# Performance work log

Measured on AMD Instinct MI355X. Metric: run time of the kernel, lower is better.

The kernel has to match this reference:

```python
import jax, jax.numpy as jnp
import numpy as np

D_MODEL = 1024
D_STATE = 64


def setup_inputs() -> dict:
    key = jax.random.key(0)
    k_x, k_a, k_b, k_c, k_d = jax.random.split(key, 5)
    x = jax.random.normal(k_x, (4, 4096, D_MODEL), dtype=jnp.float32)
    # parameter init mirrors _init_parameters
    A_diag = jax.random.uniform(k_a, (D_STATE,), minval=-0.5, maxval=0.5, dtype=jnp.float32)
    def xavier(k, shape):
        fan_in, fan_out = shape
        limit = float(np.sqrt(6.0 / (fan_in + fan_out)))
        return jax.random.uniform(k, shape, minval=-limit, maxval=limit, dtype=jnp.float32)
    B = xavier(k_b, (D_MODEL, D_STATE))
    C = xavier(k_c, (D_STATE, D_MODEL))
    D = xavier(k_d, (D_MODEL, D_MODEL)) * 0.1
    return {"x": x, "A_diag": A_diag, "B": B, "C": C, "D": D}


def reference(x, A_diag, B, C, D):
    # h_t = sigmoid(A_diag) * h_{t-1} + x_t @ B ; y_t = h_t @ C + x_t @ D
    # dropout is identity in eval mode.
    a = jax.nn.sigmoid(A_diag)                      # [S_state]
    u = jnp.einsum('btd,ds->bts', x, B)             # precompute input drive [B,T,S]

    def step(h, u_t):                               # h: [B,S], u_t: [B,S]
        h = a * h + u_t
        return h, h

    h0 = jnp.zeros((x.shape[0], A_diag.shape[0]), dtype=x.dtype)
    _, hs = jax.lax.scan(step, h0, jnp.swapaxes(u, 0, 1))  # hs: [T,B,S]
    hs = jnp.swapaxes(hs, 0, 1)                            # [B,T,S]
    y = jnp.einsum('bts,sd->btd', hs, C) + jnp.einsum('btd,de->bte', x, D)
    return y
```

## Files before the change

kernel.cpp:

```cpp
#include <hip/hip_runtime.h>
#include <hip/hip_bf16.h>

using bf16x8 = __attribute__((ext_vector_type(8))) __bf16;
using f32x4  = __attribute__((ext_vector_type(4))) float;

#define MTOT   16384
#define DMODEL 1024
#define DSTATE 64
#define KBIG   1088

__device__ __forceinline__ ushort f2b(float f) {
  __hip_bfloat16 h = __float2bfloat16(f);
  return *reinterpret_cast<ushort*>(&h);
}

__device__ __forceinline__ void gld_lds16(const ushort* g, const char* l) {
  using gptr_t = const __attribute__((address_space(1))) uint32_t*;
  using lptr_t = __attribute__((address_space(3))) uint32_t*;
  __builtin_amdgcn_global_load_lds(
      reinterpret_cast<gptr_t>(reinterpret_cast<uintptr_t>(g)),
      reinterpret_cast<lptr_t>(static_cast<uint32_t>(reinterpret_cast<uintptr_t>(l))),
      16, 0, 0);
}

#define BARRIER() do { asm volatile("" ::: "memory"); __builtin_amdgcn_s_barrier(); asm volatile("" ::: "memory"); } while (0)
#define VMCNT8() asm volatile("s_waitcnt vmcnt(8)" ::: "memory")
#define VMCNT0() asm volatile("s_waitcnt vmcnt(0)" ::: "memory")

__global__ __launch_bounds__(256) void prep_wb(const float* __restrict__ A_diag,
    const float* __restrict__ B, const float* __restrict__ C, const float* __restrict__ D,
    ushort* __restrict__ Wt, ushort* __restrict__ Btu, float* __restrict__ aSig) {
  __shared__ float tile[64][65];
  int bid = blockIdx.x;
  int tid = threadIdx.x;
  int r = tid >> 2;
  if (bid < 272) {
    int bk = bid % 17, bn = bid / 17;
    int k0 = bk * 64, n0 = bn * 64;
    const float* srow = (k0 + r < DSTATE)
        ? (C + (size_t)(k0 + r) * DMODEL + n0)
        : (D + (size_t)(k0 + r - DSTATE) * DMODEL + n0);
#pragma unroll
    for (int it = 0; it < 4; ++it) {
      int c4 = (tid & 3) + it * 4;
      float4 v = *reinterpret_cast<const float4*>(srow + c4 * 4);
      tile[r][c4 * 4 + 0] = v.x; tile[r][c4 * 4 + 1] = v.y;
      tile[r][c4 * 4 + 2] = v.z; tile[r][c4 * 4 + 3] = v.w;
    }
    __syncthreads();
#pragma unroll
    for (int it = 0; it < 2; ++it) {
      int gq = (tid & 3) + it * 4;
      ushort o[8];
#pragma unroll
      for (int j = 0; j < 8; ++j) o[j] = f2b(tile[gq * 8 + j][r]);
      *reinterpret_cast<uint4*>(&Wt[(size_t)(n0 + r) * KBIG + k0 + gq * 8]) =
          *reinterpret_cast<uint4*>(o);
    }
  } else {
    int k0 = (bid - 272) * 64;
    const float* srow = B + (size_t)(k0 + r) * DSTATE;
#pragma unroll
    for (int it = 0; it < 4; ++it) {
      int c4 = (tid & 3) + it * 4;
      float4 v = *reinterpret_cast<const float4*>(srow + c4 * 4);
      tile[r][c4 * 4 + 0] = v.x; tile[r][c4 * 4 + 1] = v.y;
      tile[r][c4 * 4 + 2] = v.z; tile[r][c4 * 4 + 3] = v.w;
    }
    __syncthreads();
#pragma unroll
    for (int it = 0; it < 2; ++it) {
      int gq = (tid & 3) + it * 4;
      ushort o[8];
#pragma unroll
      for (int j = 0; j < 8; ++j) o[j] = f2b(tile[gq * 8 + j][r]);
      *reinterpret_cast<uint4*>(&Btu[(size_t)r * DMODEL + k0 + gq * 8]) =
          *reinterpret_cast<uint4*>(o);
    }
    if (bid == 272 && tid < DSTATE) aSig[tid] = 1.0f / (1.0f + expf(-A_diag[tid]));
  }
}

__global__ __launch_bounds__(256) void fused_xu(const float* __restrict__ x,
    const ushort* __restrict__ Btu, const float* __restrict__ aSig,
    ushort* __restrict__ Z, float* __restrict__ Uloc, float* __restrict__ carry) {
  __shared__ ushort As[16][136];
  __shared__ float  Ul[16][68];
  int tid = threadIdx.x;
  int w = tid >> 6, lane = tid & 63;
  int l16 = lane & 15, lh = lane >> 4;
  int row0 = blockIdx.x * 16;
  int r = tid >> 4, kq = tid & 15;

  f32x4 acc = {};
  const float* srcBase = x + (size_t)(row0 + r) * 1024 + kq * 8;
  float4 xv0 = *reinterpret_cast<const float4*>(srcBase);
  float4 xv1 = *reinterpret_cast<const float4*>(srcBase + 4);
  for (int c = 0; c < 8; ++c) {
    int k0 = c * 128;
    ushort o[8] = {f2b(xv0.x), f2b(xv0.y), f2b(xv0.z), f2b(xv0.w),
                   f2b(xv1.x), f2b(xv1.y), f2b(xv1.z), f2b(xv1.w)};
    uint4 pk = *reinterpret_cast<uint4*>(o);
    *reinterpret_cast<uint4*>(&Z[(size_t)(row0 + r) * KBIG + DSTATE + k0 + kq * 8]) = pk;
    *reinterpret_cast<uint4*>(&As[r][kq * 8]) = pk;
    __syncthreads();
    if (c < 7) {
      const float* src = srcBase + k0 + 128;
      xv0 = *reinterpret_cast<const float4*>(src);
      xv1 = *reinterpret_cast<const float4*>(src + 4);
    }
#pragma unroll
    for (int ks = 0; ks < 4; ++ks) {
      bf16x8 af = *reinterpret_cast<const bf16x8*>(&As[l16][ks * 32 + lh * 8]);
      bf16x8 bf = *reinterpret_cast<const bf16x8*>(
          &Btu[(size_t)(w * 16 + l16) * 1024 + k0 + ks * 32 + lh * 8]);
      acc = __builtin_amdgcn_mfma_f32_16x16x32_bf16(af, bf, acc, 0, 0, 0);
    }
    __syncthreads();
  }
#pragma unroll
  for (int j = 0; j < 4; ++j)
    Ul[lh * 4 + j][w * 16 + l16] = acc[j];
  __syncthreads();
  if (w == 0) {
    int g = blockIdx.x;
    float as = aSig[lane];
    float h = 0.0f;
#pragma unroll
    for (int i = 0; i < 16; ++i) {
      h = fmaf(as, h, Ul[i][lane]);
      Uloc[(size_t)(g * 16 + i) * 64 + lane] = h;
    }
    carry[(size_t)g * 64 + lane] = h;
  }
}

__global__ __launch_bounds__(128) void scan_fix2(const float* __restrict__ aSig,
    const float* __restrict__ Uloc, const float* __restrict__ carry,
    ushort* __restrict__ Z) {
  int w = threadIdx.x >> 6, s = threadIdx.x & 63;
  int g = blockIdx.x * 2 + w;
  int b = g >> 8, c = g & 255;
  float as = aSig[s];
  float aL = as;
#pragma unroll
  for (int q = 0; q < 4; ++q) aL *= aL;
  const float* cb = carry + ((size_t)b << 8) * 64 + s;
  float H = 0.0f;
  for (int c0 = 0; c0 < 256; c0 += 16) {
    if (c0 >= c) break;
    float v[16];
#pragma unroll
    for (int i = 0; i < 16; ++i) v[i] = cb[(size_t)(c0 + i) * 64];
#pragma unroll
    for (int i = 0; i < 16; ++i)
      if (c0 + i < c) H = fmaf(aL, H, v[i]);
  }
  float p = as;
  size_t ubase = (size_t)g * 16 * 64 + s;
  size_t zbase = (size_t)(g * 16) * KBIG + s;
#pragma unroll
  for (int i = 0; i < 16; ++i) {
    float h = fmaf(p, H, Uloc[ubase + (size_t)i * 64]);
    p *= as;
    Z[zbase + (size_t)i * KBIG] = f2b(h);
  }
}

__global__ __launch_bounds__(256, 2) void gemm128(const ushort* __restrict__ A, int lda,
                                                  const ushort* __restrict__ Bt, int ldb,
                                                  float* __restrict__ Cc, int ldc, int K) {
  extern __shared__ __align__(128) char smem[];
  const int tid = threadIdx.x;
  const int wid = tid >> 6, lane = tid & 63;
  const int wm = wid >> 1, wn = wid & 1;
  const int l16 = lane & 15, lh = lane >> 4;

  int bid = blockIdx.x;
  int swz = (bid & 7) * ((int)gridDim.x >> 3) + (bid >> 3);
  const int bmRow = (swz >> 3) * 128;
  const int bnCol = (swz & 7) * 128;
  const int NT = K / 64;

  const int cswz = ((lh ^ (l16 & 7)) << 4);
  const int sRow = lane >> 3;
  const int sCol = (((lane & 7) ^ (lane >> 3)) << 3);

  const ushort* aBase = A + (size_t)(bmRow + wid * 8 + sRow) * lda + sCol;
  const ushort* bBase = Bt + (size_t)(bnCol + wid * 8 + sRow) * ldb + sCol;

  f32x4 acc[4][4] = {};
  bf16x8 aR[8], bR[8];

  auto stageA = [&](int buf, int t) {
    const ushort* g = aBase + (size_t)t * 64;
    char* d = smem + buf * 32768 + (wid * 8) * 128;
#pragma unroll
    for (int h = 0; h < 4; ++h)
      gld_lds16(g + (size_t)(h * 32) * lda, d + h * 32 * 128);
  };
  auto stageB = [&](int buf, int t) {
    const ushort* g = bBase + (size_t)t * 64;
    char* d = smem + buf * 32768 + 16384 + (wid * 8) * 128;
#pragma unroll
    for (int h = 0; h < 4; ++h)
      gld_lds16(g + (size_t)(h * 32) * ldb, d + h * 32 * 128);
  };
  auto readA = [&](int buf) {
#pragma unroll
    for (int m = 0; m < 4; ++m)
#pragma unroll
      for (int ks = 0; ks < 2; ++ks)
        aR[m * 2 + ks] = *reinterpret_cast<const bf16x8*>(
            smem + buf * 32768 + (wm * 64 + m * 16 + l16) * 128 + (cswz ^ (ks * 64)));
  };
  auto readB = [&](int buf) {
#pragma unroll
    for (int n = 0; n < 4; ++n)
#pragma unroll
      for (int ks = 0; ks < 2; ++ks)
        bR[n * 2 + ks] = *reinterpret_cast<const bf16x8*>(
            smem + buf * 32768 + 16384 + (wn * 64 + n * 16 + l16) * 128 + (cswz ^ (ks * 64)));
  };

  stageA(0, 0); stageB(0, 0);
  stageA(1, 1); stageB(1, 1);
  VMCNT8();
  BARRIER();

  for (int t = 0; t < NT; ++t) {
    const int buf = t & 1;
    const bool st2 = (t + 2 < NT);
    readA(buf); readB(buf);
    BARRIER();
    if (st2) { stageA(buf, t + 2); stageB(buf, t + 2); }
    __builtin_amdgcn_s_setprio(1);
#pragma unroll
    for (int ks = 0; ks < 2; ++ks)
#pragma unroll
      for (int m = 0; m < 4; ++m)
#pragma unroll
        for (int n = 0; n < 4; ++n)
          acc[m][n] = __builtin_amdgcn_mfma_f32_16x16x32_bf16(
              aR[m * 2 + ks], bR[n * 2 + ks], acc[m][n], 0, 0, 0);
    __builtin_amdgcn_s_setprio(0);
    if (st2) { VMCNT8(); } else { VMCNT0(); }
    BARRIER();
  }

#pragma unroll
  for (int m = 0; m < 4; ++m)
#pragma unroll
    for (int n = 0; n < 4; ++n)
#pragma unroll
      for (int j = 0; j < 4; ++j) {
        int r = bmRow + wm * 64 + m * 16 + lh * 4 + j;
        int c = bnCol + wn * 64 + n * 16 + l16;
        Cc[(size_t)r * ldc + c] = acc[m][n][j];
      }
}

extern "C" void kernel_launch(void* const* d_in, const int* in_sizes, int n_in,
                              void* d_out, int out_size, void* d_ws, size_t ws_size,
                              hipStream_t stream) {
  const float* x      = (const float*)d_in[0];
  const float* A_diag = (const float*)d_in[1];
  const float* B      = (const float*)d_in[2];
  const float* C      = (const float*)d_in[3];
  const float* D      = (const float*)d_in[4];
  float* y = (float*)d_out;

  char* w = (char*)d_ws;
  ushort* Z     = (ushort*)(w);
  ushort* Wt    = (ushort*)(w + 35651584);
  ushort* Btu   = (ushort*)(w + 37879808);
  float*  Uloc  = (float*) (w + 38010880);
  float*  carry = (float*) (w + 42205184);
  float*  aSig  = (float*) (w + 42467328);

  (void)hipFuncSetAttribute(reinterpret_cast<const void*>(&gemm128),
                            hipFuncAttributeMaxDynamicSharedMemorySize, 65536);

  prep_wb<<<dim3(288), dim3(256), 0, stream>>>(A_diag, B, C, D, Wt, Btu, aSig);
  fused_xu<<<dim3(1024), dim3(256), 0, stream>>>(x, Btu, aSig, Z, Uloc, carry);
  scan_fix2<<<dim3(512), dim3(128), 0, stream>>>(aSig, Uloc, carry, Z);
  gemm128<<<dim3(128 * 8), dim3(256), 65536, stream>>>(Z, KBIG, Wt, KBIG, y, DMODEL, KBIG);
}
```

Measured before the change: 82.71 us.

## Replace 128x128 GEMM with 256x256 tile, 8-wave ping-pong pipelined kernel

The final GEMM moves from 128x128 tiles with 4 waves to 256x256 tiles with 8 waves per block, using 128KB of LDS. It splits each K-step into four quadrant MFMA phases, and the half-tile global-to-LDS loads for the next steps are interleaved between them. The goal is better operand reuse per byte loaded and overlap of loads with MFMA work. The cost is only 256 blocks, which is roughly one wave of blocks on the device, plus many more barriers per iteration.

```diff
diff --git a/kernel.cpp b/kernel.cpp
--- a/kernel.cpp
+++ b/kernel.cpp
@@ -24,7 +24,7 @@
 }
 
 #define BARRIER() do { asm volatile("" ::: "memory"); __builtin_amdgcn_s_barrier(); asm volatile("" ::: "memory"); } while (0)
-#define VMCNT8() asm volatile("s_waitcnt vmcnt(8)" ::: "memory")
+#define VMCNT6() asm volatile("s_waitcnt vmcnt(6)" ::: "memory")
 #define VMCNT0() asm volatile("s_waitcnt vmcnt(0)" ::: "memory")
 
 __global__ __launch_bounds__(256) void prep_wb(const float* __restrict__ A_diag,
@@ -167,19 +167,19 @@
   }
 }
 
-__global__ __launch_bounds__(256, 2) void gemm128(const ushort* __restrict__ A, int lda,
-                                                  const ushort* __restrict__ Bt, int ldb,
-                                                  float* __restrict__ Cc, int ldc, int K) {
+__global__ __launch_bounds__(512) void gemm256(const ushort* __restrict__ A, int lda,
+                                               const ushort* __restrict__ Bt, int ldb,
+                                               float* __restrict__ Cc, int ldc, int K) {
   extern __shared__ __align__(128) char smem[];
   const int tid = threadIdx.x;
   const int wid = tid >> 6, lane = tid & 63;
-  const int wm = wid >> 1, wn = wid & 1;
+  const int wm = wid >> 2, wn = wid & 3;
   const int l16 = lane & 15, lh = lane >> 4;
 
   int bid = blockIdx.x;
   int swz = (bid & 7) * ((int)gridDim.x >> 3) + (bid >> 3);
-  const int bmRow = (swz >> 3) * 128;
-  const int bnCol = (swz & 7) * 128;
+  const int bmRow = (swz >> 2) * 256;
+  const int bnCol = (swz & 3) * 256;
   const int NT = K / 64;
 
   const int cswz = ((lh ^ (l16 & 7)) << 4);
@@ -189,74 +189,122 @@
   const ushort* aBase = A + (size_t)(bmRow + wid * 8 + sRow) * lda + sCol;
   const ushort* bBase = Bt + (size_t)(bnCol + wid * 8 + sRow) * ldb + sCol;
 
-  f32x4 acc[4][4] = {};
-  bf16x8 aR[8], bR[8];
-
-  auto stageA = [&](int buf, int t) {
-    const ushort* g = aBase + (size_t)t * 64;
-    char* d = smem + buf * 32768 + (wid * 8) * 128;
-#pragma unroll
-    for (int h = 0; h < 4; ++h)
-      gld_lds16(g + (size_t)(h * 32) * lda, d + h * 32 * 128);
-  };
-  auto stageB = [&](int buf, int t) {
-    const ushort* g = bBase + (size_t)t * 64;
-    char* d = smem + buf * 32768 + 16384 + (wid * 8) * 128;
-#pragma unroll
-    for (int h = 0; h < 4; ++h)
-      gld_lds16(g + (size_t)(h * 32) * ldb, d + h * 32 * 128);
-  };
-  auto readA = [&](int buf) {
+  f32x4 acc[8][4] = {};
+  bf16x8 a0[8], a1[8], b0[4], b1[4];
+
+  auto stageAH = [&](int buf, int t, int h) {
+    const ushort* g = aBase + (size_t)(h * 128) * lda + (size_t)t * 64;
+    const char* d = smem + buf * 65536 + (h * 128 + wid * 8) * 128;
+    gld_lds16(g, d);
+    gld_lds16(g + (size_t)64 * lda, d + 64 * 128);
+  };
+  auto stageBH = [&](int buf, int t, int h) {
+    const ushort* g = bBase + (size_t)(h * 128) * ldb + (size_t)t * 64;
+    const char* d = smem + buf * 65536 + 32768 + (h * 128 + wid * 8) * 128;
+    gld_lds16(g, d);
+    gld_lds16(g + (size_t)64 * ldb, d + 64 * 128);
+  };
+  auto readA = [&](bf16x8 (&dst)[8], int buf, int qm) {
 #pragma unroll
     for (int m = 0; m < 4; ++m)
 #pragma unroll
       for (int ks = 0; ks < 2; ++ks)
-        aR[m * 2 + ks] = *reinterpret_cast<const bf16x8*>(
-            smem + buf * 32768 + (wm * 64 + m * 16 + l16) * 128 + (cswz ^ (ks * 64)));
-  };
-  auto readB = [&](int buf) {
-#pragma unroll
-    for (int n = 0; n < 4; ++n)
+        dst[m * 2 + ks] = *reinterpret_cast<const bf16x8*>(
+            smem + buf * 65536 + (wm * 128 + qm * 64 + m * 16 + l16) * 128 + (cswz ^ (ks * 64)));
+  };
+  auto readB = [&](bf16x8 (&dst)[4], int buf, int qn) {
+#pragma unroll
+    for (int n = 0; n < 2; ++n)
 #pragma unroll
       for (int ks = 0; ks < 2; ++ks)
-        bR[n * 2 + ks] = *reinterpret_cast<const bf16x8*>(
-            smem + buf * 32768 + 16384 + (wn * 64 + n * 16 + l16) * 128 + (cswz ^ (ks * 64)));
-  };
-
-  stageA(0, 0); stageB(0, 0);
-  stageA(1, 1); stageB(1, 1);
-  VMCNT8();
-  BARRIER();
-
-  for (int t = 0; t < NT; ++t) {
-    const int buf = t & 1;
-    const bool st2 = (t + 2 < NT);
-    readA(buf); readB(buf);
-    BARRIER();
-    if (st2) { stageA(buf, t + 2); stageB(buf, t + 2); }
+        dst[n * 2 + ks] = *reinterpret_cast<const bf16x8*>(
+            smem + buf * 65536 + 32768 + (wn * 64 + qn * 32 + n * 16 + l16) * 128 + (cswz ^ (ks * 64)));
+  };
+  auto mfmaQ = [&](bf16x8 (&a8)[8], bf16x8 (&b4)[4], int qm, int qn) {
     __builtin_amdgcn_s_setprio(1);
 #pragma unroll
     for (int ks = 0; ks < 2; ++ks)
 #pragma unroll
       for (int m = 0; m < 4; ++m)
 #pragma unroll
-        for (int n = 0; n < 4; ++n)
-          acc[m][n] = __builtin_amdgcn_mfma_f32_16x16x32_bf16(
-              aR[m * 2 + ks], bR[n * 2 + ks], acc[m][n], 0, 0, 0);
+        for (int n = 0; n < 2; ++n)
+          acc[qm * 4 + m][qn * 2 + n] = __builtin_amdgcn_mfma_f32_16x16x32_bf16(
+              a8[m * 2 + ks], b4[n * 2 + ks], acc[qm * 4 + m][qn * 2 + n], 0, 0, 0);
     __builtin_amdgcn_s_setprio(0);
-    if (st2) { VMCNT8(); } else { VMCNT0(); }
-    BARRIER();
-  }
-
-#pragma unroll
-  for (int m = 0; m < 4; ++m)
-#pragma unroll
-    for (int n = 0; n < 4; ++n)
+  };
+
+  stageBH(0, 0, 0); stageBH(0, 0, 1); stageAH(0, 0, 0); stageAH(0, 0, 1);
+  stageBH(1, 1, 0); stageBH(1, 1, 1); stageAH(1, 1, 0);
+  VMCNT6();
+  BARRIER();
+
+  for (int t = 0; t + 2 < NT; t += 2) {
+    const bool s3 = (t + 3 < NT);
+    readA(a0, 0, 0); readB(b0, 0, 0);
+    stageAH(1, t + 1, 1);
+    BARRIER();
+    mfmaQ(a0, b0, 0, 0);
+    BARRIER();
+    readB(b1, 0, 1);
+    stageBH(0, t + 2, 0);
+    BARRIER();
+    mfmaQ(a0, b1, 0, 1);
+    BARRIER();
+    readA(a1, 0, 1);
+    stageBH(0, t + 2, 1);
+    BARRIER();
+    mfmaQ(a1, b0, 1, 0);
+    BARRIER();
+    stageAH(0, t + 2, 0);
+    BARRIER();
+    mfmaQ(a1, b1, 1, 1);
+    VMCNT6();
+    BARRIER();
+    readA(a0, 1, 0); readB(b0, 1, 0);
+    stageAH(0, t + 2, 1);
+    BARRIER();
+    mfmaQ(a0, b0, 0, 0);
+    BARRIER();
+    readB(b1, 1, 1);
+    if (s3) stageBH(1, t + 3, 0);
+    BARRIER();
+    mfmaQ(a0, b1, 0, 1);
+    BARRIER();
+    readA(a1, 1, 1);
+    if (s3) stageBH(1, t + 3, 1);
+    BARRIER();
+    mfmaQ(a1, b0, 1, 0);
+    BARRIER();
+    if (s3) stageAH(1, t + 3, 0);
+    BARRIER();
+    mfmaQ(a1, b1, 1, 1);
+    if (s3) { VMCNT6(); } else { VMCNT0(); }
+    BARRIER();
+  }
+
+  readA(a0, 0, 0); readB(b0, 0, 0);
+  BARRIER();
+  mfmaQ(a0, b0, 0, 0);
+  BARRIER();
+  readB(b1, 0, 1);
+  BARRIER();
+  mfmaQ(a0, b1, 0, 1);
+  BARRIER();
+  readA(a1, 0, 1);
+  BARRIER();
+  mfmaQ(a1, b0, 1, 0);
+  BARRIER();
+  mfmaQ(a1, b1, 1, 1);
+
+#pragma unroll
+  for (int i = 0; i < 8; ++i)
+#pragma unroll
+    for (int jn = 0; jn < 4; ++jn)
 #pragma unroll
       for (int j = 0; j < 4; ++j) {
-        int r = bmRow + wm * 64 + m * 16 + lh * 4 + j;
-        int c = bnCol + wn * 64 + n * 16 + l16;
-        Cc[(size_t)r * ldc + c] = acc[m][n][j];
+        int r = bmRow + wm * 128 + (i >> 2) * 64 + (i & 3) * 16 + lh * 4 + j;
+        int c = bnCol + wn * 64 + (jn >> 1) * 32 + (jn & 1) * 16 + l16;
+        Cc[(size_t)r * ldc + c] = acc[i][jn][j];
       }
 }
 
@@ -278,11 +326,11 @@
   float*  carry = (float*) (w + 42205184);
   float*  aSig  = (float*) (w + 42467328);
 
-  (void)hipFuncSetAttribute(reinterpret_cast<const void*>(&gemm128),
-                            hipFuncAttributeMaxDynamicSharedMemorySize, 65536);
+  (void)hipFuncSetAttribute(reinterpret_cast<const void*>(&gemm256),
+                            hipFuncAttributeMaxDynamicSharedMemorySize, 131072);
 
   prep_wb<<<dim3(288), dim3(256), 0, stream>>>(A_diag, B, C, D, Wt, Btu, aSig);
   fused_xu<<<dim3(1024), dim3(256), 0, stream>>>(x, Btu, aSig, Z, Uloc, carry);
   scan_fix2<<<dim3(512), dim3(128), 0, stream>>>(aSig, Uloc, carry, Z);
-  gemm128<<<dim3(128 * 8), dim3(256), 65536, stream>>>(Z, KBIG, Wt, KBIG, y, DMODEL, KBIG);
-}
+  gemm256<<<dim3(64 * 4), dim3(512), 131072, stream>>>(Z, KBIG, Wt, KBIG, y, DMODEL, KBIG);
+}
```

Measured after the change: 86.52 us. +4.6%, slower.
